# Kernel tuning notes

Hardware: AMD Instinct MI355X
Metric: run time of the kernel (lower is better)

The kernel has to match this reference:

```python
import jax, jax.numpy as jnp
import numpy as np

B, N, D = 16, 512, 256
PH, UH, UPH = 8, 4, 4          # P_GAT heads, U_GAT heads, UP_GAT heads
P_LAYERS, U_LAYERS = 2, 1
FH, NC = 128, 2                # final hidden, num classes
N_TRAIT = 4


def setup_inputs() -> dict:
    key = jax.random.key(0)
    keys = iter(jax.random.split(key, 64))

    def rn(shape, s=0.05):
        return jax.random.normal(next(keys), shape, dtype=jnp.float32) * s

    inp = {
        "p_mask": jnp.ones((B, N), jnp.float32),
        "feature": rn((B, N, D), 1.0),
        "c_node": rn((B, 1, D), 1.0),
        "pgat_W": rn((D, D)),
        "pgat_attn": rn((PH, 2 * (D // PH))),
    }
    for i in range(1, 5):
        inp[f"up{i}_qw"] = rn((D, D))
        inp[f"up{i}_qb"] = rn((D,))
        inp[f"up{i}_kw"] = rn((D, D))
        inp[f"up{i}_kb"] = rn((D,))
        inp[f"up{i}_ow"] = rn((D, D * UPH))
        inp[f"up{i}_ob"] = rn((D,))
    inp["ugat_W"] = rn((D, D))
    inp["ugat_attn"] = rn((UH, 2 * (D // UH)))
    inp["mlp_w1"] = rn((FH, D))
    inp["mlp_b1"] = rn((FH,))
    inp["mlp_w2"] = rn((FH, FH))
    inp["mlp_b2"] = rn((FH,))
    for i in range(1, 5):
        inp[f"fcf{i}_w"] = rn((NC, FH))
        inp[f"fcf{i}_b"] = rn((NC,))
    return inp


def _mh_gat(feature, W, attn_w, n_head, num_layers, adj=None):
    """Shared math of P_GAT / U_GAT.
    attn(cat([q_i, k_j]))[..., h, h] decomposes into q_i.wq_h + k_j.wk_h,
    identical math to the broadcast-concat-linear-diagonal in the source."""
    Bx, Nx, d = feature.shape
    dh = d // n_head
    wq, wk = attn_w[:, :dh], attn_w[:, dh:]           # [h, dh] each
    for _ in range(num_layers):
        qk = (feature @ W.T).reshape(Bx, Nx, n_head, dh)
        sq = jnp.einsum('bqhd,hd->bqh', qk, wq)
        sk = jnp.einsum('bkhd,hd->bkh', qk, wk)
        scores = jnp.tanh(sq[:, :, None, :] + sk[:, None, :, :])  # [B,q,k,h]
        if adj is not None:
            scores = jnp.where(adj[:, :, :, None] == 0, jnp.float32(-1e-8), scores)
        att = jax.nn.softmax(scores, axis=-2)          # softmax over k
        hid = jnp.tanh(jnp.einsum('bqkh,bkhd->bqhd', att, qk))
        feature = feature + hid.reshape(Bx, Nx, d)
    return feature


def _up_gat(p_mask, p_feat, u_feat, qw, qb, kw, kb, ow, ob):
    """UP_GAT: all heads/layers share params & inputs -> identical heads."""
    d = p_feat.shape[-1]
    q = u_feat @ qw.T + qb                             # [B,1,D]
    k = p_feat @ kw.T + kb                             # [B,Np,D]
    sim = jnp.einsum('bqd,bkd->bqk', q, k) / jnp.sqrt(jnp.float32(d))
    sim = jnp.where(p_mask[:, None, :] == 0, jnp.float32(1e-8), sim)
    att = jax.nn.softmax(sim, axis=2)
    head = att @ p_feat                                # [B,1,D]
    mh = jnp.concatenate([head] * UPH, axis=-1)        # concat of identical heads
    return (mh @ ow.T + ob)[:, 0, :]                   # squeeze(1)


def reference(p_mask, feature, c_node, pgat_W, pgat_attn,
              up1_qw, up1_qb, up1_kw, up1_kb, up1_ow, up1_ob,
              up2_qw, up2_qb, up2_kw, up2_kb, up2_ow, up2_ob,
              up3_qw, up3_qb, up3_kw, up3_kb, up3_ow, up3_ob,
              up4_qw, up4_qb, up4_kw, up4_kb, up4_ow, up4_ob,
              ugat_W, ugat_attn, mlp_w1, mlp_b1, mlp_w2, mlp_b2,
              fcf1_w, fcf1_b, fcf2_w, fcf2_b, fcf3_w, fcf3_b, fcf4_w, fcf4_b):
    Bx = p_mask.shape[0]
    adj = p_mask[:, :, None] * p_mask[:, None, :]      # [B,N,N]
    new_p = _mh_gat(feature, pgat_W, pgat_attn, PH, P_LAYERS, adj=adj)
    new_mask = jnp.concatenate([p_mask, jnp.ones((Bx, 1), p_mask.dtype)], axis=1)
    comb = jnp.concatenate([new_p, c_node], axis=1)    # [B,N+1,D]

    u1 = _up_gat(new_mask, comb, c_node, up1_qw, up1_qb, up1_kw, up1_kb, up1_ow, up1_ob)
    u2 = _up_gat(new_mask, comb, c_node, up2_qw, up2_qb, up2_kw, up2_kb, up2_ow, up2_ob)
    u3 = _up_gat(new_mask, comb, c_node, up3_qw, up3_qb, up3_kw, up3_kb, up3_ow, up3_ob)
    u4 = _up_gat(new_mask, comb, c_node, up4_qw, up4_qb, up4_kw, up4_kb, up4_ow, up4_ob)

    u = jnp.stack([u1, u2, u3, u4], axis=1)            # [B,4,D]
    u = _mh_gat(u, ugat_W, ugat_attn, UH, U_LAYERS, adj=None)

    def mlp(x):  # fcs1..4 share modules in the torch source
        h = jax.nn.relu(x @ mlp_w1.T + mlp_b1)
        return jax.nn.relu(h @ mlp_w2.T + mlp_b2)

    heads = [(fcf1_w, fcf1_b), (fcf2_w, fcf2_b), (fcf3_w, fcf3_b), (fcf4_w, fcf4_b)]
    logits = [mlp(u[:, i]) @ w.T + b for i, (w, b) in enumerate(heads)]
    return jnp.stack(logits, axis=0)                   # [4,B,NC]
```

## Files before the change

### kernel.cpp

```cpp
#include <hip/hip_runtime.h>

constexpr int CB   = 16;
constexpr int CN   = 512;
constexpr int CD   = 256;
constexpr int CPH  = 8;
constexpr int CDH  = 32;
constexpr int CNP1 = 513;
constexpr int CFH  = 128;
constexpr int CNC  = 2;

typedef __bf16 bf16x8 __attribute__((ext_vector_type(8)));
typedef __bf16 bf16x4 __attribute__((ext_vector_type(4)));
typedef float  f32x4  __attribute__((ext_vector_type(4)));

__device__ __forceinline__ float tanh_fast(float x) {
  x = fminf(fmaxf(x, -15.f), 15.f);
  float e = __expf(2.f * x);
  return (e - 1.f) / (e + 1.f);
}

__device__ __forceinline__ float exp2x_clamped(float x) {
  x = fminf(fmaxf(x, -18.f), 18.f);
  return __expf(2.f * x);
}

__global__ __launch_bounds__(256) void gemm_fused(
    const float* __restrict__ A, const float* __restrict__ W,
    const float* __restrict__ attnw, __bf16* __restrict__ C,
    float* __restrict__ sqT, float* __restrict__ skT,
    const float* __restrict__ cnode,
    const float* __restrict__ qw0, const float* __restrict__ qb0,
    const float* __restrict__ kw0, const float* __restrict__ kb0,
    const float* __restrict__ ow0,
    const float* __restrict__ qw1, const float* __restrict__ qb1,
    const float* __restrict__ kw1, const float* __restrict__ kb1,
    const float* __restrict__ ow1,
    const float* __restrict__ qw2, const float* __restrict__ qb2,
    const float* __restrict__ kw2, const float* __restrict__ kb2,
    const float* __restrict__ ow2,
    const float* __restrict__ qw3, const float* __restrict__ qb3,
    const float* __restrict__ kw3, const float* __restrict__ kb3,
    const float* __restrict__ ow3,
    float* __restrict__ qt_, float* __restrict__ qkb,
    float* __restrict__ comb, float* __restrict__ head, float* __restrict__ den,
    float* __restrict__ weff)
{
  const int t  = threadIdx.x;

  __shared__ __align__(16) __bf16 aHi[64][56];
  __shared__ __align__(16) __bf16 aLo[64][56];
  __shared__ __align__(16) __bf16 bHi[64][56];
  __shared__ __align__(16) __bf16 bLo[64][56];
  __shared__ float s_cl[CD];
  __shared__ float s_ql[CD];
  __shared__ float s_red[256];

  if (blockIdx.y >= 128) {
    const int up = blockIdx.x, b = blockIdx.y - 128;
    const float* qw = (up == 0) ? qw0 : (up == 1) ? qw1 : (up == 2) ? qw2 : qw3;
    const float* qb = (up == 0) ? qb0 : (up == 1) ? qb1 : (up == 2) ? qb2 : qb3;
    const float* kw = (up == 0) ? kw0 : (up == 1) ? kw1 : (up == 2) ? kw2 : kw3;
    const float* kb = (up == 0) ? kb0 : (up == 1) ? kb1 : (up == 2) ? kb2 : kb3;
    const float* ow = (up == 0) ? ow0 : (up == 1) ? ow1 : (up == 2) ? ow2 : ow3;
    s_cl[t] = cnode[b * CD + t];
    head[((size_t)b * 4 + up) * CD + t] = 0.f;
    if (t == 0) den[b * 4 + up] = 0.f;

    {
#pragma unroll
      for (int i = 0; i < 4; i++) {
        int idx = t + 256 * i;
        int n = b * 16 + (idx >> 6), e4 = (idx & 63) * 4;
        const float* base = ow + (size_t)n * (4 * CD) + e4;
        float4 w0 = *(const float4*)(base);
        float4 w1 = *(const float4*)(base + CD);
        float4 w2 = *(const float4*)(base + 2 * CD);
        float4 w3 = *(const float4*)(base + 3 * CD);
        float4 o;
        o.x = w0.x + w1.x + w2.x + w3.x;
        o.y = w0.y + w1.y + w2.y + w3.y;
        o.z = w0.z + w1.z + w2.z + w3.z;
        o.w = w0.w + w1.w + w2.w + w3.w;
        *(float4*)(weff + (size_t)up * CD * CD + (size_t)n * CD + e4) = o;
      }
    }
    __syncthreads();
    if (up == 0) comb[((size_t)b * CNP1 + CN) * CD + t] = s_cl[t];
    {
      const float* wr = qw + (size_t)t * CD;
      float a = qb[t];
#pragma unroll 4
      for (int k = 0; k < CD; k += 4) {
        float4 w4 = *(const float4*)(wr + k);
        a += s_cl[k] * w4.x + s_cl[k + 1] * w4.y + s_cl[k + 2] * w4.z + s_cl[k + 3] * w4.w;
      }
      s_ql[t] = a;
    }
    __syncthreads();
    {
      float a0 = 0.f, a1 = 0.f, a2 = 0.f, a3 = 0.f;
#pragma unroll 4
      for (int d = 0; d < CD; d += 4) {
        a0 += s_ql[d]     * kw[(d)     * CD + t];
        a1 += s_ql[d + 1] * kw[(d + 1) * CD + t];
        a2 += s_ql[d + 2] * kw[(d + 2) * CD + t];
        a3 += s_ql[d + 3] * kw[(d + 3) * CD + t];
      }
      qt_[((size_t)up * CB + b) * CD + t] = (a0 + a1) + (a2 + a3);
    }
    s_red[t] = s_ql[t] * kb[t];
    __syncthreads();
    for (int s = 128; s > 0; s >>= 1) { if (t < s) s_red[t] += s_red[t + s]; __syncthreads(); }
    if (t == 0) qkb[up * CB + b] = s_red[0];
    return;
  }

  const int nt = blockIdx.x * 64;
  const int mt = blockIdx.y * 64;
  const int wv = t >> 6, ln = t & 63;
  const int quad = ln >> 4, lc = ln & 15;

  f32x4 acc[4];
#pragma unroll
  for (int j = 0; j < 4; j++)
#pragma unroll
    for (int r = 0; r < 4; r++) acc[j][r] = 0.f;

  const int sr  = t >> 2;
  const int skq = (t & 3) * 8;

  for (int k0 = 0; k0 < 256; k0 += 32) {
    __syncthreads();
    {
      const float* ap = A + (size_t)(mt + sr) * 256 + k0 + skq;
      const float* wp = W + (size_t)(nt + sr) * 256 + k0 + skq;
      float4 a0 = *(const float4*)ap, a1 = *(const float4*)(ap + 4);
      float4 w0 = *(const float4*)wp, w1 = *(const float4*)(wp + 4);
      float av[8] = {a0.x, a0.y, a0.z, a0.w, a1.x, a1.y, a1.z, a1.w};
      float wvv[8] = {w0.x, w0.y, w0.z, w0.w, w1.x, w1.y, w1.z, w1.w};
      bf16x8 ah, al, bh, bl;
#pragma unroll
      for (int j = 0; j < 8; j++) {
        ah[j] = (__bf16)av[j];
        al[j] = (__bf16)(av[j] - (float)ah[j]);
        bh[j] = (__bf16)wvv[j];
        bl[j] = (__bf16)(wvv[j] - (float)bh[j]);
      }
      *(bf16x8*)&aHi[sr][skq] = ah;
      *(bf16x8*)&aLo[sr][skq] = al;
      *(bf16x8*)&bHi[sr][skq] = bh;
      *(bf16x8*)&bLo[sr][skq] = bl;
    }
    __syncthreads();
    bf16x8 fah = *(const bf16x8*)&aHi[wv * 16 + lc][quad * 8];
    bf16x8 fal = *(const bf16x8*)&aLo[wv * 16 + lc][quad * 8];
#pragma unroll
    for (int j = 0; j < 4; j++) {
      bf16x8 fbh = *(const bf16x8*)&bHi[j * 16 + lc][quad * 8];
      bf16x8 fbl = *(const bf16x8*)&bLo[j * 16 + lc][quad * 8];
      acc[j] = __builtin_amdgcn_mfma_f32_16x16x32_bf16(fah, fbh, acc[j], 0, 0, 0);
      acc[j] = __builtin_amdgcn_mfma_f32_16x16x32_bf16(fah, fbl, acc[j], 0, 0, 0);
      acc[j] = __builtin_amdgcn_mfma_f32_16x16x32_bf16(fal, fbh, acc[j], 0, 0, 0);
    }
  }
#pragma unroll
  for (int j = 0; j < 4; j++)
#pragma unroll
    for (int r = 0; r < 4; r++)
      C[(size_t)(mt + wv * 16 + quad * 4 + r) * 256 + nt + j * 16 + lc] =
          (__bf16)acc[j][r];

  const int hA = blockIdx.x * 2, hB = hA + 1;
  const float wqa0 = attnw[hA * 64 + lc],      wqa1 = attnw[hA * 64 + 16 + lc];
  const float wka0 = attnw[hA * 64 + 32 + lc], wka1 = attnw[hA * 64 + 48 + lc];
  const float wqb0 = attnw[hB * 64 + lc],      wqb1 = attnw[hB * 64 + 16 + lc];
  const float wkb0 = attnw[hB * 64 + 32 + lc], wkb1 = attnw[hB * 64 + 48 + lc];
  float sqa[4], ska[4], sqb[4], skb[4];
#pragma unroll
  for (int r = 0; r < 4; r++) {
    sqa[r] = acc[0][r] * wqa0 + acc[1][r] * wqa1;
    ska[r] = acc[0][r] * wka0 + acc[1][r] * wka1;
    sqb[r] = acc[2][r] * wqb0 + acc[3][r] * wqb1;
    skb[r] = acc[2][r] * wkb0 + acc[3][r] * wkb1;
  }
#pragma unroll
  for (int m = 1; m <= 8; m <<= 1) {
#pragma unroll
    for (int r = 0; r < 4; r++) {
      sqa[r] += __shfl_xor(sqa[r], m);
      ska[r] += __shfl_xor(ska[r], m);
      sqb[r] += __shfl_xor(sqb[r], m);
      skb[r] += __shfl_xor(skb[r], m);
    }
  }
  if (lc == 0) {
#pragma unroll
    for (int r = 0; r < 4; r++) {
      int gm = mt + wv * 16 + quad * 4 + r;
      int bb = gm >> 9, nn = gm & 511;
      sqT[((size_t)bb * CPH + hA) * CN + nn] = sqa[r];
      skT[((size_t)bb * CPH + hA) * CN + nn] = ska[r];
      sqT[((size_t)bb * CPH + hB) * CN + nn] = sqb[r];
      skT[((size_t)bb * CPH + hB) * CN + nn] = skb[r];
    }
  }
}

__global__ __launch_bounds__(256) void pgat_attn_mfma2(
    const __bf16* __restrict__ qk, const float* __restrict__ sqT,
    const float* __restrict__ skT, const float* __restrict__ pmask,
    const float* __restrict__ fin, float* __restrict__ fout, int outStride)
{
  const int qt = blockIdx.x;
  const int h  = blockIdx.y;
  const int b  = blockIdx.z;
  const int t  = threadIdx.x;
  const int wv = t >> 6;
  const int ln = t & 63;
  const int quad = ln >> 4;
  const int lc   = ln & 15;

  __shared__ __align__(16) __bf16 pbuf[128][72];
  __shared__ __align__(16) __bf16 vbuf[32][72];
  __shared__ float skl[CN];
  __shared__ float ckm[CN];
  __shared__ float sql[128];
  __shared__ float qfm[128];

  for (int i = t; i < CN; i += 256) {
    skl[i] = exp2x_clamped(skT[((size_t)b * CPH + h) * CN + i]);
    ckm[i] = (pmask[b * CN + i] == 0.f) ? 0.f : 1.f;
  }
  if (t < 128) {
    sql[t] = exp2x_clamped(sqT[((size_t)b * CPH + h) * CN + qt * 128 + t]);
    qfm[t] = (pmask[b * CN + qt * 128 + t] == 0.f) ? 0.f : 1.f;
  }

  f32x4 aV0 = {0.f,0.f,0.f,0.f}, aV1 = {0.f,0.f,0.f,0.f}, aD = {0.f,0.f,0.f,0.f};
  f32x4 bV0 = {0.f,0.f,0.f,0.f}, bV1 = {0.f,0.f,0.f,0.f}, bD = {0.f,0.f,0.f,0.f};
  bf16x8 ones;
#pragma unroll
  for (int j = 0; j < 8; j++) ones[j] = (__bf16)1.0f;

  const int qg  = t >> 1;
  const int kb  = (t & 1) * 32;
  const int vkk = t >> 3;
  const int vdq = (t & 7) * 4;

  for (int k0 = 0; k0 < CN; k0 += 64) {
    __syncthreads();
    {
      bf16x4 v0 = *(const bf16x4*)(qk + ((size_t)(b * CN + k0 + vkk)) * CD + h * CDH + vdq);
      bf16x4 v1 = *(const bf16x4*)(qk + ((size_t)(b * CN + k0 + 32 + vkk)) * CD + h * CDH + vdq);
      vbuf[vdq + 0][vkk] = v0[0]; vbuf[vdq + 1][vkk] = v0[1];
      vbuf[vdq + 2][vkk] = v0[2]; vbuf[vdq + 3][vkk] = v0[3];
      vbuf[vdq + 0][32 + vkk] = v1[0]; vbuf[vdq + 1][32 + vkk] = v1[1];
      vbuf[vdq + 2][32 + vkk] = v1[2]; vbuf[vdq + 3][32 + vkk] = v1[3];
    }
    {
      const float tq = sql[qg];
      const float qf = qfm[qg];
#pragma unroll
      for (int g = 0; g < 4; g++) {
        bf16x8 w;
#pragma unroll
        for (int j = 0; j < 8; j++) {
          const int kk = k0 + kb + g * 8 + j;
          float u  = tq * skl[kk];
          float th = (u - 1.f) * __builtin_amdgcn_rcpf(u + 1.f);
          th *= qf * ckm[kk];
          w[j] = (__bf16)__expf(th);
        }
        *(bf16x8*)&pbuf[qg][kb + g * 8] = w;
      }
    }
    __syncthreads();
#pragma unroll
    for (int s = 0; s < 2; s++) {
      bf16x8 b0 = *(const bf16x8*)&vbuf[lc][s * 32 + quad * 8];
      bf16x8 b1 = *(const bf16x8*)&vbuf[16 + lc][s * 32 + quad * 8];
      bf16x8 fa = *(const bf16x8*)&pbuf[wv * 16 + lc][s * 32 + quad * 8];
      bf16x8 fb = *(const bf16x8*)&pbuf[64 + wv * 16 + lc][s * 32 + quad * 8];
      aV0 = __builtin_amdgcn_mfma_f32_16x16x32_bf16(fa, b0, aV0, 0, 0, 0);
      aV1 = __builtin_amdgcn_mfma_f32_16x16x32_bf16(fa, b1, aV1, 0, 0, 0);
      aD  = __builtin_amdgcn_mfma_f32_16x16x32_bf16(fa, ones, aD, 0, 0, 0);
      bV0 = __builtin_amdgcn_mfma_f32_16x16x32_bf16(fb, b0, bV0, 0, 0, 0);
      bV1 = __builtin_amdgcn_mfma_f32_16x16x32_bf16(fb, b1, bV1, 0, 0, 0);
      bD  = __builtin_amdgcn_mfma_f32_16x16x32_bf16(fb, ones, bD, 0, 0, 0);
    }
  }
#pragma unroll
  for (int r = 0; r < 4; r++) {
    const int d0 = h * CDH + lc;
    {
      int q = qt * 128 + wv * 16 + quad * 4 + r;
      float inv = 1.f / aD[r];
      const float* ip = fin + ((size_t)b * CN + q) * CD;
      float*       op = fout + ((size_t)b * outStride + q) * CD;
      op[d0]      = ip[d0]      + tanh_fast(aV0[r] * inv);
      op[d0 + 16] = ip[d0 + 16] + tanh_fast(aV1[r] * inv);
    }
    {
      int q = qt * 128 + 64 + wv * 16 + quad * 4 + r;
      float inv = 1.f / bD[r];
      const float* ip = fin + ((size_t)b * CN + q) * CD;
      float*       op = fout + ((size_t)b * outStride + q) * CD;
      op[d0]      = ip[d0]      + tanh_fast(bV0[r] * inv);
      op[d0 + 16] = ip[d0 + 16] + tanh_fast(bV1[r] * inv);
    }
  }
}


__global__ __launch_bounds__(256) void up_headsim(
    const float* __restrict__ comb, const float* __restrict__ qt,
    const float* __restrict__ qkb, const float* __restrict__ pmask,
    float* __restrict__ head, float* __restrict__ den)
{
  const int b = blockIdx.x, n0 = blockIdx.y * 64, t = threadIdx.x;
  const int up = t >> 6, j = t & 63;
  __shared__ float qtl[4][CD];
  __shared__ float qkbl[4];
  __shared__ float attl[4][64];
  for (int i = t; i < 4 * CD; i += 256)
    qtl[i >> 8][i & 255] = qt[((size_t)(i >> 8) * CB + b) * CD + (i & 255)];
  if (t < 4) qkbl[t] = qkb[t * CB + b];
  __syncthreads();
  {
    const int n = n0 + j;
    float e = 0.f;
    if (n < CNP1) {
      const float* cr = comb + ((size_t)b * CNP1 + n) * CD;
      float p = 0.f;
#pragma unroll 4
      for (int d = 0; d < CD; d += 4) {
        float4 c4 = *(const float4*)(cr + d);
        p += qtl[up][d] * c4.x + qtl[up][d + 1] * c4.y
           + qtl[up][d + 2] * c4.z + qtl[up][d + 3] * c4.w;
      }
      float s = (p + qkbl[up]) * 0.0625f;
      float m = (n < CN) ? pmask[b * CN + n] : 1.f;
      if (m == 0.f) s = 1e-8f;
      e = __expf(s);
    }
    attl[up][j] = e;
  }
  __syncthreads();
  float4 acc = make_float4(0.f, 0.f, 0.f, 0.f);
  const int nmax = min(64, CNP1 - n0);
  for (int jj = 0; jj < nmax; jj++) {
    float a = attl[up][jj];
    float4 c4 = *(const float4*)(comb + ((size_t)b * CNP1 + n0 + jj) * CD + j * 4);
    acc.x += a * c4.x; acc.y += a * c4.y; acc.z += a * c4.z; acc.w += a * c4.w;
  }
  float* hp = head + ((size_t)b * 4 + up) * CD + j * 4;
  atomicAdd(hp + 0, acc.x); atomicAdd(hp + 1, acc.y);
  atomicAdd(hp + 2, acc.z); atomicAdd(hp + 3, acc.w);
  if (j == 0) {
    float s = 0.f;
    for (int jj = 0; jj < 64; jj++) s += attl[up][jj];
    atomicAdd(den + b * 4 + up, s);
  }
}

__global__ __launch_bounds__(256) void up_out_ugat(
    const float* __restrict__ head, const float* __restrict__ den,
    const float* __restrict__ weff,
    const float* __restrict__ ob0, const float* __restrict__ ob1,
    const float* __restrict__ ob2, const float* __restrict__ ob3,
    const float* __restrict__ ugat_W, const float* __restrict__ attnw,
    float* __restrict__ uout, float* __restrict__ uqk, float* __restrict__ sqk)
{
  const int b = blockIdx.x, up = blockIdx.y, t = threadIdx.x;
  const float* ob = (up == 0) ? ob0 : (up == 1) ? ob1 : (up == 2) ? ob2 : ob3;
  __shared__ float hl[CD];
  __shared__ float xl[CD];
  __shared__ float qkl[CD];
  hl[t] = head[((size_t)b * 4 + up) * CD + t] * (1.f / den[b * 4 + up]);
  __syncthreads();
  {
    const float* r0 = weff + (size_t)up * CD * CD + (size_t)t * CD;
    float p0 = 0.f, p1 = 0.f, p2 = 0.f, p3 = 0.f;
#pragma unroll 4
    for (int d = 0; d < CD; d += 16) {
      float4 w0 = *(const float4*)(r0 + d);
      float4 w1 = *(const float4*)(r0 + d + 4);
      float4 w2 = *(const float4*)(r0 + d + 8);
      float4 w3 = *(const float4*)(r0 + d + 12);
      p0 += hl[d +  0] * w0.x + hl[d +  1] * w0.y + hl[d +  2] * w0.z + hl[d +  3] * w0.w;
      p1 += hl[d +  4] * w1.x + hl[d +  5] * w1.y + hl[d +  6] * w1.z + hl[d +  7] * w1.w;
      p2 += hl[d +  8] * w2.x + hl[d +  9] * w2.y + hl[d + 10] * w2.z + hl[d + 11] * w2.w;
      p3 += hl[d + 12] * w3.x + hl[d + 13] * w3.y + hl[d + 14] * w3.z + hl[d + 15] * w3.w;
    }
    float a = ob[t] + ((p0 + p1) + (p2 + p3));
    xl[t] = a;
    uout[((size_t)b * 4 + up) * CD + t] = a;
  }
  __syncthreads();
  {
    const float* wr = ugat_W + (size_t)t * CD;
    float p0 = 0.f, p1 = 0.f, p2 = 0.f, p3 = 0.f;
#pragma unroll 4
    for (int d = 0; d < CD; d += 16) {
      float4 w0 = *(const float4*)(wr + d);
      float4 w1 = *(const float4*)(wr + d + 4);
      float4 w2 = *(const float4*)(wr + d + 8);
      float4 w3 = *(const float4*)(wr + d + 12);
      p0 += xl[d +  0] * w0.x + xl[d +  1] * w0.y + xl[d +  2] * w0.z + xl[d +  3] * w0.w;
      p1 += xl[d +  4] * w1.x + xl[d +  5] * w1.y + xl[d +  6] * w1.z + xl[d +  7] * w1.w;
      p2 += xl[d +  8] * w2.x + xl[d +  9] * w2.y + xl[d + 10] * w2.z + xl[d + 11] * w2.w;
      p3 += xl[d + 12] * w3.x + xl[d + 13] * w3.y + xl[d + 14] * w3.z + xl[d + 15] * w3.w;
    }
    float a = (p0 + p1) + (p2 + p3);
    qkl[t] = a;
    uqk[((size_t)b * 4 + up) * CD + t] = a;
  }
  __syncthreads();
  if (t < 8) {
    const int h = t >> 1, which = t & 1;
    const float* w = attnw + h * 128 + which * 64;
    float s = 0.f;
    for (int j = 0; j < 64; j++) s += qkl[h * 64 + j] * w[j];
    sqk[(((size_t)b * 4 + up) * 4 + h) * 2 + which] = s;
  }
}

__global__ __launch_bounds__(256) void ugat_mlp2(
    const float* __restrict__ u, const float* __restrict__ uqk,
    const float* __restrict__ sqk,
    const float* __restrict__ w1, const float* __restrict__ b1,
    const float* __restrict__ w2, const float* __restrict__ b2,
    const float* __restrict__ f1w, const float* __restrict__ f1b,
    const float* __restrict__ f2w, const float* __restrict__ f2b,
    const float* __restrict__ f3w, const float* __restrict__ f3b,
    const float* __restrict__ f4w, const float* __restrict__ f4b,
    float* __restrict__ out)
{
  const int b = blockIdx.x, trait = blockIdx.y, t = threadIdx.x;
  __shared__ float uq[4][CD];
  __shared__ float sl[4][4], kl[4][4];
  __shared__ float xl[CD];
  __shared__ float h1[CFH];
  __shared__ float h2[CFH];
  for (int i = t; i < 4 * CD; i += 256) uq[i >> 8][i & 255] = uqk[(size_t)b * 4 * CD + i];
  if (t < 16) {
    int node = t >> 2, h = t & 3;
    sl[node][h] = sqk[(((size_t)b * 4 + node) * 4 + h) * 2 + 0];
    kl[node][h] = sqk[(((size_t)b * 4 + node) * 4 + h) * 2 + 1];
  }
  float ur = u[((size_t)b * 4 + trait) * CD + t];
  __syncthreads();
  {
    const int h = t >> 6;
    float e[4]; float ssum = 0.f;
#pragma unroll
    for (int k = 0; k < 4; k++) { e[k] = __expf(tanh_fast(sl[trait][h] + kl[k][h])); ssum += e[k]; }
    float hid = 0.f;
#pragma unroll
    for (int k = 0; k < 4; k++) hid += e[k] * uq[k][t];
    xl[t] = ur + tanh_fast(hid / ssum);
  }
  __syncthreads();
  if (t < CFH) {
    const float* r = w1 + (size_t)t * CD;
    float a = b1[t];
#pragma unroll 4
    for (int k = 0; k < CD; k += 4) {
      float4 v = *(const float4*)(r + k);
      a += xl[k] * v.x + xl[k + 1] * v.y + xl[k + 2] * v.z + xl[k + 3] * v.w;
    }
    h1[t] = fmaxf(a, 0.f);
  }
  __syncthreads();
  if (t < CFH) {
    const float* r = w2 + (size_t)t * CFH;
    float a = b2[t];
#pragma unroll 4
    for (int k = 0; k < CFH; k += 4) {
      float4 v = *(const float4*)(r + k);
      a += h1[k] * v.x + h1[k + 1] * v.y + h1[k + 2] * v.z + h1[k + 3] * v.w;
    }
    h2[t] = fmaxf(a, 0.f);
  }
  __syncthreads();
  if (t < CNC) {
    const float* fw; const float* fb;
    switch (trait) {
      case 0:  fw = f1w; fb = f1b; break;
      case 1:  fw = f2w; fb = f2b; break;
      case 2:  fw = f3w; fb = f3b; break;
      default: fw = f4w; fb = f4b; break;
    }
    const float* r = fw + (size_t)t * CFH;
    float a = fb[t];
    for (int k = 0; k < CFH; k++) a += h2[k] * r[k];
    out[(size_t)trait * (CB * CNC) + b * CNC + t] = a;
  }
}

extern "C" void kernel_launch(void* const* d_in, const int* in_sizes, int n_in,
                              void* d_out, int out_size, void* d_ws, size_t ws_size,
                              hipStream_t stream) {
  (void)in_sizes; (void)n_in; (void)out_size; (void)ws_size;
  const float* pmask    = (const float*)d_in[0];
  const float* feature  = (const float*)d_in[1];
  const float* cnode    = (const float*)d_in[2];
  const float* pgat_W   = (const float*)d_in[3];
  const float* pgat_att = (const float*)d_in[4];
  const float* upw[4][6];
  for (int i = 0; i < 4; i++)
    for (int j = 0; j < 6; j++) upw[i][j] = (const float*)d_in[5 + i * 6 + j];
  const float* ugat_W   = (const float*)d_in[29];
  const float* ugat_att = (const float*)d_in[30];
  const float* mlp_w1 = (const float*)d_in[31];
  const float* mlp_b1 = (const float*)d_in[32];
  const float* mlp_w2 = (const float*)d_in[33];
  const float* mlp_b2 = (const float*)d_in[34];
  const float* fcf[8];
  for (int j = 0; j < 8; j++) fcf[j] = (const float*)d_in[35 + j];

  float* ws = (float*)d_ws;
  size_t o = 0;
  float* ws_qk   = ws + o; o += (size_t)CB * CN * CD;
  float* ws_feat = ws + o; o += (size_t)CB * CN * CD;
  float* ws_comb = ws + o; o += (size_t)CB * CNP1 * CD;
  float* ws_sq   = ws + o; o += (size_t)CB * CPH * CN;
  float* ws_sk   = ws + o; o += (size_t)CB * CPH * CN;
  float* ws_qt   = ws + o; o += (size_t)4 * CB * CD;
  float* ws_qkb  = ws + o; o += 4 * CB;
  float* ws_den  = ws + o; o += CB * 4;
  float* ws_head = ws + o; o += (size_t)CB * 4 * CD;
  float* ws_u    = ws + o; o += (size_t)CB * 4 * CD;
  float* ws_uqk  = ws + o; o += (size_t)CB * 4 * CD;
  float* ws_sqk  = ws + o; o += (size_t)CB * 4 * 4 * 2;
  float* ws_weff = ws + o; o += (size_t)4 * CD * CD;
  __bf16* qk16 = (__bf16*)ws_qk;

  const dim3 gemmGrid1(CD / 64, (CB * CN) / 64 + 16);
  const dim3 gemmGrid2(CD / 64, (CB * CN) / 64);
  const dim3 attnGrid(CN / 128, CPH, CB);

  gemm_fused<<<gemmGrid1, 256, 0, stream>>>(feature, pgat_W, pgat_att, qk16, ws_sq, ws_sk,
      cnode,
      upw[0][0], upw[0][1], upw[0][2], upw[0][3], upw[0][4],
      upw[1][0], upw[1][1], upw[1][2], upw[1][3], upw[1][4],
      upw[2][0], upw[2][1], upw[2][2], upw[2][3], upw[2][4],
      upw[3][0], upw[3][1], upw[3][2], upw[3][3], upw[3][4],
      ws_qt, ws_qkb, ws_comb, ws_head, ws_den, ws_weff);
  pgat_attn_mfma2<<<attnGrid, 256, 0, stream>>>(qk16, ws_sq, ws_sk, pmask, feature, ws_feat, CN);
  gemm_fused<<<gemmGrid2, 256, 0, stream>>>(ws_feat, pgat_W, pgat_att, qk16, ws_sq, ws_sk,
      cnode,
      upw[0][0], upw[0][1], upw[0][2], upw[0][3], upw[0][4],
      upw[1][0], upw[1][1], upw[1][2], upw[1][3], upw[1][4],
      upw[2][0], upw[2][1], upw[2][2], upw[2][3], upw[2][4],
      upw[3][0], upw[3][1], upw[3][2], upw[3][3], upw[3][4],
      ws_qt, ws_qkb, ws_comb, ws_head, ws_den, ws_weff);
  pgat_attn_mfma2<<<attnGrid, 256, 0, stream>>>(qk16, ws_sq, ws_sk, pmask, ws_feat, ws_comb, CNP1);

  up_headsim<<<dim3(CB, (CNP1 + 63) / 64), 256, 0, stream>>>(ws_comb, ws_qt, ws_qkb, pmask,
                                                             ws_head, ws_den);
  up_out_ugat<<<dim3(CB, 4), 256, 0, stream>>>(ws_head, ws_den, ws_weff,
      upw[0][5], upw[1][5], upw[2][5], upw[3][5],
      ugat_W, ugat_att, ws_u, ws_uqk, ws_sqk);

  ugat_mlp2<<<dim3(CB, 4), 256, 0, stream>>>(ws_u, ws_uqk, ws_sqk,
                                             mlp_w1, mlp_b1, mlp_w2, mlp_b2,
                                             fcf[0], fcf[1], fcf[2], fcf[3],
                                             fcf[4], fcf[5], fcf[6], fcf[7],
                                             (float*)d_out);
}
```

Baseline: 267.3 us.

## Pre-split weight into bf16 hi/lo fragment layout and drop LDS staging in GEMM

Adds a small prep kernel that splits pgat_W once into bf16 hi/lo parts, stored in the exact MFMA fragment order. The GEMM then loads B fragments straight from global memory and builds A fragments per lane from registers, removing the shared-memory tiles and both __syncthreads per k-step. This removes the redundant weight conversion in every block and the LDS round trip. The cost is one extra launch and B fragments read from L2/global without reuse through LDS.

```diff
diff --git a/kernel.cpp b/kernel.cpp
--- a/kernel.cpp
+++ b/kernel.cpp
@@ -24,8 +24,31 @@
   return __expf(2.f * x);
 }
 
+__global__ __launch_bounds__(256) void prep_wsplit(
+    const float* __restrict__ W, bf16x8* __restrict__ wfH, bf16x8* __restrict__ wfL)
+{
+  const int id = blockIdx.x * 256 + threadIdx.x;
+  const int row = id >> 5;
+  const int c   = id & 31;
+  const float* src = W + (size_t)row * CD + c * 8;
+  float4 a0 = *(const float4*)src, a1 = *(const float4*)(src + 4);
+  float v[8] = {a0.x, a0.y, a0.z, a0.w, a1.x, a1.y, a1.z, a1.w};
+  bf16x8 hi, lo;
+#pragma unroll
+  for (int j = 0; j < 8; j++) {
+    hi[j] = (__bf16)v[j];
+    lo[j] = (__bf16)(v[j] - (float)hi[j]);
+  }
+  const int x = row >> 6, jj = (row >> 4) & 3, lc = row & 15;
+  const int s = c >> 2, q = c & 3;
+  const int idx = (((x * 8 + s) * 4 + jj) * 4 + q) * 16 + lc;
+  wfH[idx] = hi;
+  wfL[idx] = lo;
+}
+
 __global__ __launch_bounds__(256) void gemm_fused(
-    const float* __restrict__ A, const float* __restrict__ W,
+    const float* __restrict__ A,
+    const bf16x8* __restrict__ wfH, const bf16x8* __restrict__ wfL,
     const float* __restrict__ attnw, __bf16* __restrict__ C,
     float* __restrict__ sqT, float* __restrict__ skT,
     const float* __restrict__ cnode,
@@ -47,10 +70,6 @@
 {
   const int t  = threadIdx.x;
 
-  __shared__ __align__(16) __bf16 aHi[64][56];
-  __shared__ __align__(16) __bf16 aLo[64][56];
-  __shared__ __align__(16) __bf16 bHi[64][56];
-  __shared__ __align__(16) __bf16 bLo[64][56];
   __shared__ float s_cl[CD];
   __shared__ float s_ql[CD];
   __shared__ float s_red[256];
@@ -115,7 +134,8 @@
     return;
   }
 
-  const int nt = blockIdx.x * 64;
+  const int x  = blockIdx.x;
+  const int nt = x * 64;
   const int mt = blockIdx.y * 64;
   const int wv = t >> 6, ln = t & 63;
   const int quad = ln >> 4, lc = ln & 15;
@@ -126,41 +146,27 @@
 #pragma unroll
     for (int r = 0; r < 4; r++) acc[j][r] = 0.f;
 
-  const int sr  = t >> 2;
-  const int skq = (t & 3) * 8;
-
-  for (int k0 = 0; k0 < 256; k0 += 32) {
-    __syncthreads();
-    {
-      const float* ap = A + (size_t)(mt + sr) * 256 + k0 + skq;
-      const float* wp = W + (size_t)(nt + sr) * 256 + k0 + skq;
-      float4 a0 = *(const float4*)ap, a1 = *(const float4*)(ap + 4);
-      float4 w0 = *(const float4*)wp, w1 = *(const float4*)(wp + 4);
-      float av[8] = {a0.x, a0.y, a0.z, a0.w, a1.x, a1.y, a1.z, a1.w};
-      float wvv[8] = {w0.x, w0.y, w0.z, w0.w, w1.x, w1.y, w1.z, w1.w};
-      bf16x8 ah, al, bh, bl;
-#pragma unroll
-      for (int j = 0; j < 8; j++) {
-        ah[j] = (__bf16)av[j];
-        al[j] = (__bf16)(av[j] - (float)ah[j]);
-        bh[j] = (__bf16)wvv[j];
-        bl[j] = (__bf16)(wvv[j] - (float)bh[j]);
-      }
-      *(bf16x8*)&aHi[sr][skq] = ah;
-      *(bf16x8*)&aLo[sr][skq] = al;
-      *(bf16x8*)&bHi[sr][skq] = bh;
-      *(bf16x8*)&bLo[sr][skq] = bl;
-    }
-    __syncthreads();
-    bf16x8 fah = *(const bf16x8*)&aHi[wv * 16 + lc][quad * 8];
-    bf16x8 fal = *(const bf16x8*)&aLo[wv * 16 + lc][quad * 8];
+  const float* ap = A + (size_t)(mt + wv * 16 + lc) * CD + quad * 8;
+
+#pragma unroll 2
+  for (int s = 0; s < 8; s++) {
+    float4 a0 = *(const float4*)(ap + s * 32);
+    float4 a1 = *(const float4*)(ap + s * 32 + 4);
+    float av[8] = {a0.x, a0.y, a0.z, a0.w, a1.x, a1.y, a1.z, a1.w};
+    bf16x8 ah, al;
+#pragma unroll
+    for (int j = 0; j < 8; j++) {
+      ah[j] = (__bf16)av[j];
+      al[j] = (__bf16)(av[j] - (float)ah[j]);
+    }
+    const int base = ((x * 8 + s) * 16 + quad) * 16 + lc;
 #pragma unroll
     for (int j = 0; j < 4; j++) {
-      bf16x8 fbh = *(const bf16x8*)&bHi[j * 16 + lc][quad * 8];
-      bf16x8 fbl = *(const bf16x8*)&bLo[j * 16 + lc][quad * 8];
-      acc[j] = __builtin_amdgcn_mfma_f32_16x16x32_bf16(fah, fbh, acc[j], 0, 0, 0);
-      acc[j] = __builtin_amdgcn_mfma_f32_16x16x32_bf16(fah, fbl, acc[j], 0, 0, 0);
-      acc[j] = __builtin_amdgcn_mfma_f32_16x16x32_bf16(fal, fbh, acc[j], 0, 0, 0);
+      bf16x8 bh = wfH[base + j * 64];
+      bf16x8 bl = wfL[base + j * 64];
+      acc[j] = __builtin_amdgcn_mfma_f32_16x16x32_bf16(ah, bh, acc[j], 0, 0, 0);
+      acc[j] = __builtin_amdgcn_mfma_f32_16x16x32_bf16(ah, bl, acc[j], 0, 0, 0);
+      acc[j] = __builtin_amdgcn_mfma_f32_16x16x32_bf16(al, bh, acc[j], 0, 0, 0);
     }
   }
 #pragma unroll
@@ -534,13 +540,19 @@
   float* ws_uqk  = ws + o; o += (size_t)CB * 4 * CD;
   float* ws_sqk  = ws + o; o += (size_t)CB * 4 * 4 * 2;
   float* ws_weff = ws + o; o += (size_t)4 * CD * CD;
+  float* ws_wfh  = ws + o; o += (size_t)CD * CD / 2;
+  float* ws_wfl  = ws + o; o += (size_t)CD * CD / 2;
   __bf16* qk16 = (__bf16*)ws_qk;
+  bf16x8* wfH = (bf16x8*)ws_wfh;
+  bf16x8* wfL = (bf16x8*)ws_wfl;
 
   const dim3 gemmGrid1(CD / 64, (CB * CN) / 64 + 16);
   const dim3 gemmGrid2(CD / 64, (CB * CN) / 64);
   const dim3 attnGrid(CN / 128, CPH, CB);
 
-  gemm_fused<<<gemmGrid1, 256, 0, stream>>>(feature, pgat_W, pgat_att, qk16, ws_sq, ws_sk,
+  prep_wsplit<<<dim3(32), 256, 0, stream>>>(pgat_W, wfH, wfL);
+
+  gemm_fused<<<gemmGrid1, 256, 0, stream>>>(feature, wfH, wfL, pgat_att, qk16, ws_sq, ws_sk,
       cnode,
       upw[0][0], upw[0][1], upw[0][2], upw[0][3], upw[0][4],
       upw[1][0], upw[1][1], upw[1][2], upw[1][3], upw[1][4],
@@ -548,7 +560,7 @@
       upw[3][0], upw[3][1], upw[3][2], upw[3][3], upw[3][4],
       ws_qt, ws_qkb, ws_comb, ws_head, ws_den, ws_weff);
   pgat_attn_mfma2<<<attnGrid, 256, 0, stream>>>(qk16, ws_sq, ws_sk, pmask, feature, ws_feat, CN);
-  gemm_fused<<<gemmGrid2, 256, 0, stream>>>(ws_feat, pgat_W, pgat_att, qk16, ws_sq, ws_sk,
+  gemm_fused<<<gemmGrid2, 256, 0, stream>>>(ws_feat, wfH, wfL, pgat_att, qk16, ws_sq, ws_sk,
       cnode,
       upw[0][0], upw[0][1], upw[0][2], upw[0][3], upw[0][4],
       upw[1][0], upw[1][1], upw[1][2], upw[1][3], upw[1][4],
```

Result: no change. 267.7 us (+0.2%).
